# Performance work log

Hardware: AMD Instinct MI355X
Metric: run time of the kernel (lower is better)

The kernel has to match this reference:

```python
import jax, jax.numpy as jnp
import numpy as np

NUM_HEADS = 16
LN_EPS = 1e-5


def setup_inputs() -> dict:
    key = jax.random.key(0)
    ks = jax.random.split(key, 6)
    b, s, d = 2, 2048, 1024
    scale = 1.0 / np.sqrt(d)
    return {
        "x": jax.random.normal(ks[0], (b, s, d), dtype=jnp.float32),
        "W_w": jax.random.normal(ks[1], (3 * d, d), dtype=jnp.float32) * scale,
        "W_b": jax.random.normal(ks[2], (3 * d,), dtype=jnp.float32) * 0.01,
        "proj_w": jax.random.normal(ks[3], (d, d), dtype=jnp.float32) * scale,
        "proj_b": jax.random.normal(ks[4], (d,), dtype=jnp.float32) * 0.01,
        "gamma": jnp.ones((d,), dtype=jnp.float32),
        "beta": jnp.zeros((d,), dtype=jnp.float32),
    }


def reference(x, W_w, W_b, proj_w, proj_b, gamma, beta):
    b, s, d = x.shape
    h = NUM_HEADS
    hd = d // h
    # fused QKV projection: [b,s,3d]
    qkv = x @ W_w.T + W_b
    q, k, v = jnp.split(qkv, 3, axis=-1)
    # [b,s,d] -> [b,h,s,hd]
    q, k, v = (z.reshape(b, s, h, hd).transpose(0, 2, 1, 3) for z in (q, k, v))
    # NOTE: original scales by sqrt(d), not sqrt(head_dim)
    attn = jnp.einsum('bhqd,bhkd->bhqk', q, k) / jnp.sqrt(jnp.asarray(d, x.dtype))
    attn_weights = jax.nn.softmax(attn, axis=-1)  # [b,h,s,s]
    o = jnp.einsum('bhqk,bhkd->bhqd', attn_weights, v)
    o = o.transpose(0, 2, 1, 3).reshape(b, s, d)
    out = o @ proj_w.T + proj_b  # dropout is identity at eval
    y = x + out
    mu = jnp.mean(y, axis=-1, keepdims=True)
    var = jnp.var(y, axis=-1, keepdims=True)
    y_norm = (y - mu) / jnp.sqrt(var + LN_EPS) * gamma + beta
    return (y_norm, attn_weights)
```

## Files before the change

### kernel.cpp

```cpp
#include <hip/hip_runtime.h>
#include <cstdint>

#define BB 2
#define SS 2048
#define DD 1024
#define HH 16
#define HDIM 64
#define MM (BB*SS)
#define N3 (3*DD)

typedef __attribute__((ext_vector_type(4))) float f32x4;
typedef __attribute__((ext_vector_type(8))) __bf16 bf16x8;

static __device__ __forceinline__ unsigned short f2bf_fast(float f) {
  __bf16 h = (__bf16)f;
  return __builtin_bit_cast(unsigned short, h);
}

static __device__ __forceinline__ uint4 pack8f(const float4 a, const float4 b) {
  union { unsigned short us[8]; uint4 v; } pk;
  pk.us[0] = f2bf_fast(a.x); pk.us[1] = f2bf_fast(a.y); pk.us[2] = f2bf_fast(a.z); pk.us[3] = f2bf_fast(a.w);
  pk.us[4] = f2bf_fast(b.x); pk.us[5] = f2bf_fast(b.y); pk.us[6] = f2bf_fast(b.z); pk.us[7] = f2bf_fast(b.w);
  return pk.v;
}

static __device__ __forceinline__ void gload16(const unsigned short* g, unsigned short* l) {
  __builtin_amdgcn_global_load_lds(
      (const __attribute__((address_space(1))) void*)g,
      (__attribute__((address_space(3))) void*)l, 16, 0, 0);
}

__global__ __launch_bounds__(256) void cvt_kernel(
    const float* __restrict__ x, const float* __restrict__ Ww,
    const float* __restrict__ pw,
    unsigned short* __restrict__ xb, unsigned short* __restrict__ Wwb,
    unsigned short* __restrict__ pwb) {
  const size_t i = ((size_t)blockIdx.x * 256 + threadIdx.x) * 8;
  const float* src;
  unsigned short* dst;
  if (i < 4194304u)       { src = x  + i;            dst = xb  + i; }
  else if (i < 7340032u)  { src = Ww + (i - 4194304u); dst = Wwb + (i - 4194304u); }
  else                    { src = pw + (i - 7340032u); dst = pwb + (i - 7340032u); }
  const float4* s4 = (const float4*)src;
  *(uint4*)dst = pack8f(s4[0], s4[1]);
}

__global__ __launch_bounds__(256) void gemm_qkv(
    const unsigned short* __restrict__ xb, const unsigned short* __restrict__ Wwb,
    const float* __restrict__ Wb,
    unsigned short* __restrict__ qb, unsigned short* __restrict__ kb,
    unsigned short* __restrict__ vbT) {
  __shared__ __align__(16) unsigned short Sh[128 * 132];
  unsigned short* As = Sh;
  unsigned short* Bs = Sh + 128 * 32;
  const int t = threadIdx.x;
  const int l = t & 63, w = t >> 6;
  const int wr = w >> 1, wc = w & 1;
  const int m0 = blockIdx.y * 128, n0 = blockIdx.x * 128;
  f32x4 acc[4][4] = {};

  for (int kt = 0; kt < DD; kt += 32) {
    __syncthreads();
    #pragma unroll
    for (int i = 0; i < 2; ++i) {
      const int row = (i * 4 + w) * 16 + (l >> 2);
      const int cc = (l & 3) * 8;
      gload16(xb  + (size_t)(m0 + row) * DD + kt + cc, &As[(i * 4 + w) * 512]);
      gload16(Wwb + (size_t)(n0 + row) * DD + kt + cc, &Bs[(i * 4 + w) * 512]);
    }
    __syncthreads();
    bf16x8 a[4], b[4];
    #pragma unroll
    for (int i = 0; i < 4; ++i) {
      a[i] = __builtin_bit_cast(bf16x8, *(const uint4*)&As[(wr * 64 + i * 16 + (l & 15)) * 32 + (l >> 4) * 8]);
      b[i] = __builtin_bit_cast(bf16x8, *(const uint4*)&Bs[(wc * 64 + i * 16 + (l & 15)) * 32 + (l >> 4) * 8]);
    }
    #pragma unroll
    for (int i = 0; i < 4; ++i)
      #pragma unroll
      for (int j = 0; j < 4; ++j)
        acc[i][j] = __builtin_amdgcn_mfma_f32_16x16x32_bf16(a[i], b[j], acc[i][j], 0, 0, 0);
  }
  __syncthreads();

  if (n0 < 2048) {
    const bool isq = (n0 < 1024);
    #pragma unroll
    for (int i = 0; i < 4; ++i)
      #pragma unroll
      for (int j = 0; j < 4; ++j)
        #pragma unroll
        for (int r = 0; r < 4; ++r) {
          const int row = m0 + wr * 64 + i * 16 + (l >> 4) * 4 + r;
          const int col = n0 + wc * 64 + j * 16 + (l & 15);
          const float v = acc[i][j][r] + Wb[col];
          const int bidx = row >> 11, srow = row & 2047;
          const int cc = col & 1023, head = cc >> 6, hd = cc & 63;
          const size_t idx = ((size_t)((bidx * HH + head) * SS + srow)) * HDIM + hd;
          if (isq) qb[idx] = f2bf_fast(v * 0.04508422f);
          else     kb[idx] = f2bf_fast(v);
        }
  } else {
    unsigned short* Tt = Sh;
    #pragma unroll
    for (int i = 0; i < 4; ++i)
      #pragma unroll
      for (int j = 0; j < 4; ++j)
        #pragma unroll
        for (int r = 0; r < 4; ++r) {
          const int rr = wr * 64 + i * 16 + (l >> 4) * 4 + r;
          const int cl = wc * 64 + j * 16 + (l & 15);
          Tt[rr * 132 + cl] = f2bf_fast(acc[i][j][r] + Wb[n0 + cl]);
        }
    __syncthreads();
    const int bidx = m0 >> 11, srow0 = m0 & 2047;
    const int q = t & 3;
    #pragma unroll
    for (int ci = 0; ci < 2; ++ci) {
      const int c = ci * 64 + (t >> 2);
      const int vcol = n0 - 2048 + c;
      const int head = vcol >> 6, hd = vcol & 63;
      unsigned short* dst = vbT + ((size_t)(bidx * HH + head) * HDIM + hd) * SS + srow0;
      #pragma unroll
      for (int e8 = 0; e8 < 4; ++e8) {
        const int r0 = e8 * 32 + q * 8;
        union { unsigned short us[8]; uint4 v; } pk;
        #pragma unroll
        for (int e = 0; e < 8; ++e) pk.us[e] = Tt[(r0 + e) * 132 + c];
        *(uint4*)(dst + r0) = pk.v;
      }
    }
  }
}

__global__ __launch_bounds__(256) void attn_kernel(
    const unsigned short* __restrict__ qb,
    const unsigned short* __restrict__ kb,
    const unsigned short* __restrict__ vbT,
    unsigned short* __restrict__ ob,
    float* __restrict__ attn_out) {
  __shared__ float Ored[4][64][68];
  __shared__ float Lred[4][64];
  const int t = threadIdx.x;
  const int l = t & 63, w = t >> 6;
  const int q_l = l & 15, hi = l >> 4;
  const int bid = blockIdx.x;
  const int swz = (bid & 7) * 128 + (bid >> 3);
  const int bh = swz >> 5;
  const int q0 = (swz & 31) * 64;
  const size_t base = (size_t)bh * SS * HDIM;

  bf16x8 qa[4][2];
  #pragma unroll
  for (int j = 0; j < 4; ++j)
    #pragma unroll
    for (int kc = 0; kc < 2; ++kc)
      qa[j][kc] = __builtin_bit_cast(bf16x8,
          *(const uint4*)(qb + base + (size_t)(q0 + j * 16 + q_l) * HDIM + kc * 32 + hi * 8));

  const unsigned short* kga = kb + base + (size_t)(w * 16 + q_l) * HDIM + hi * 8;
  const unsigned short* vga = vbT + ((size_t)bh * HDIM + q_l) * SS + w * 16 + hi * 4;

  float lsum[4] = {0.f, 0.f, 0.f, 0.f};
  {
    uint4 k0 = *(const uint4*)(kga);
    uint4 k1 = *(const uint4*)(kga + 32);
    for (int kt = 0; kt < SS; kt += 64) {
      const bool more = (kt + 64) < SS;
      uint4 n0, n1;
      if (more) {
        n0 = *(const uint4*)(kga + (size_t)(kt + 64) * HDIM);
        n1 = *(const uint4*)(kga + (size_t)(kt + 64) * HDIM + 32);
      }
      f32x4 sQ[4] = {};
      const bf16x8 kf0 = __builtin_bit_cast(bf16x8, k0);
      const bf16x8 kf1 = __builtin_bit_cast(bf16x8, k1);
      __builtin_amdgcn_s_setprio(1);
      #pragma unroll
      for (int j = 0; j < 4; ++j) {
        sQ[j] = __builtin_amdgcn_mfma_f32_16x16x32_bf16(kf0, qa[j][0], sQ[j], 0, 0, 0);
        sQ[j] = __builtin_amdgcn_mfma_f32_16x16x32_bf16(kf1, qa[j][1], sQ[j], 0, 0, 0);
      }
      __builtin_amdgcn_s_setprio(0);
      #pragma unroll
      for (int j = 0; j < 4; ++j)
        #pragma unroll
        for (int r = 0; r < 4; ++r)
          lsum[j] += __builtin_amdgcn_exp2f(sQ[j][r]);
      k0 = n0; k1 = n1;
    }
  }
  #pragma unroll
  for (int j = 0; j < 4; ++j) {
    float s = lsum[j];
    s += __shfl_xor(s, 16);
    s += __shfl_xor(s, 32);
    lsum[j] = s;
  }
  if (hi == 0) {
    #pragma unroll
    for (int j = 0; j < 4; ++j) Lred[w][j * 16 + q_l] = lsum[j];
  }
  __syncthreads();
  float rl[4];
  #pragma unroll
  for (int j = 0; j < 4; ++j)
    rl[j] = 1.0f / (Lred[0][j * 16 + q_l] + Lred[1][j * 16 + q_l] +
                    Lred[2][j * 16 + q_l] + Lred[3][j * 16 + q_l]);

  float* pbs[4];
  #pragma unroll
  for (int j = 0; j < 4; ++j)
    pbs[j] = attn_out + ((size_t)bh * SS + (q0 + j * 16 + q_l)) * SS + w * 16 + hi * 4;

  f32x4 of[4][4] = {};
  {
    uint4 k0 = *(const uint4*)(kga);
    uint4 k1 = *(const uint4*)(kga + 32);
    uint2 vv[4];
    #pragma unroll
    for (int d4 = 0; d4 < 4; ++d4)
      vv[d4] = *(const uint2*)(vga + (size_t)(d4 * 16) * SS);
    for (int kt = 0; kt < SS; kt += 64) {
      const bool more = (kt + 64) < SS;
      uint4 n0, n1; uint2 nv[4];
      if (more) {
        n0 = *(const uint4*)(kga + (size_t)(kt + 64) * HDIM);
        n1 = *(const uint4*)(kga + (size_t)(kt + 64) * HDIM + 32);
        #pragma unroll
        for (int d4 = 0; d4 < 4; ++d4)
          nv[d4] = *(const uint2*)(vga + (size_t)(d4 * 16) * SS + kt + 64);
      }
      f32x4 sQ[4] = {};
      const bf16x8 kf0 = __builtin_bit_cast(bf16x8, k0);
      const bf16x8 kf1 = __builtin_bit_cast(bf16x8, k1);
      __builtin_amdgcn_s_setprio(1);
      #pragma unroll
      for (int j = 0; j < 4; ++j) {
        sQ[j] = __builtin_amdgcn_mfma_f32_16x16x32_bf16(kf0, qa[j][0], sQ[j], 0, 0, 0);
        sQ[j] = __builtin_amdgcn_mfma_f32_16x16x32_bf16(kf1, qa[j][1], sQ[j], 0, 0, 0);
      }
      __builtin_amdgcn_s_setprio(0);
      bf16x8 pbp[4];
      #pragma unroll
      for (int j = 0; j < 4; ++j) {
        float4 pv;
        pv.x = __builtin_amdgcn_exp2f(sQ[j][0]) * rl[j];
        pv.y = __builtin_amdgcn_exp2f(sQ[j][1]) * rl[j];
        pv.z = __builtin_amdgcn_exp2f(sQ[j][2]) * rl[j];
        pv.w = __builtin_amdgcn_exp2f(sQ[j][3]) * rl[j];
        __builtin_nontemporal_store(*(const f32x4*)&pv, (f32x4*)(pbs[j] + kt));
        union { unsigned short us[8]; uint4 v; } pk;
        pk.us[0] = f2bf_fast(pv.x); pk.us[1] = f2bf_fast(pv.y);
        pk.us[2] = f2bf_fast(pv.z); pk.us[3] = f2bf_fast(pv.w);
        pk.us[4] = 0; pk.us[5] = 0; pk.us[6] = 0; pk.us[7] = 0;
        pbp[j] = __builtin_bit_cast(bf16x8, pk.v);
      }
      __builtin_amdgcn_s_setprio(1);
      #pragma unroll
      for (int d4 = 0; d4 < 4; ++d4) {
        uint4 vp; vp.x = vv[d4].x; vp.y = vv[d4].y; vp.z = 0u; vp.w = 0u;
        const bf16x8 vfp = __builtin_bit_cast(bf16x8, vp);
        #pragma unroll
        for (int j = 0; j < 4; ++j)
          of[d4][j] = __builtin_amdgcn_mfma_f32_16x16x32_bf16(vfp, pbp[j], of[d4][j], 0, 0, 0);
      }
      __builtin_amdgcn_s_setprio(0);
      k0 = n0; k1 = n1;
      #pragma unroll
      for (int d4 = 0; d4 < 4; ++d4) vv[d4] = nv[d4];
    }
  }

  #pragma unroll
  for (int d4 = 0; d4 < 4; ++d4)
    #pragma unroll
    for (int j = 0; j < 4; ++j)
      *(f32x4*)&Ored[w][j * 16 + q_l][d4 * 16 + hi * 4] = of[d4][j];
  __syncthreads();
  const int bidx = bh >> 4, h_ = bh & 15;
  const int qf = w * 16 + q_l;
  union { unsigned short us[16]; uint4 v[2]; } opk;
  #pragma unroll
  for (int c4 = 0; c4 < 4; ++c4) {
    const int d0 = hi * 16 + c4 * 4;
    f32x4 s = *(const f32x4*)&Ored[0][qf][d0];
    s += *(const f32x4*)&Ored[1][qf][d0];
    s += *(const f32x4*)&Ored[2][qf][d0];
    s += *(const f32x4*)&Ored[3][qf][d0];
    opk.us[c4 * 4 + 0] = f2bf_fast(s[0]);
    opk.us[c4 * 4 + 1] = f2bf_fast(s[1]);
    opk.us[c4 * 4 + 2] = f2bf_fast(s[2]);
    opk.us[c4 * 4 + 3] = f2bf_fast(s[3]);
  }
  unsigned short* orow = ob + ((size_t)bidx * SS + (q0 + qf)) * DD + h_ * 64 + hi * 16;
  *(uint4*)orow = opk.v[0];
  *(uint4*)(orow + 8) = opk.v[1];
}

__global__ __launch_bounds__(256) void gemm_proj(
    const unsigned short* __restrict__ ob, const unsigned short* __restrict__ pwb,
    const float* __restrict__ pb, const float* __restrict__ x,
    float* __restrict__ y) {
  __shared__ __align__(16) unsigned short As[64 * 32];
  __shared__ __align__(16) unsigned short Bs[128 * 32];
  const int t = threadIdx.x;
  const int l = t & 63, w = t >> 6;
  const int wr = w >> 1, wc = w & 1;
  const int m0 = blockIdx.y * 64, n0 = blockIdx.x * 128;
  f32x4 acc[2][4] = {};

  for (int kt = 0; kt < DD; kt += 32) {
    __syncthreads();
    {
      const int rowA = w * 16 + (l >> 2);
      const int cc = (l & 3) * 8;
      gload16(ob + (size_t)(m0 + rowA) * DD + kt + cc, &As[w * 512]);
      #pragma unroll
      for (int i = 0; i < 2; ++i) {
        const int rowB = (i * 4 + w) * 16 + (l >> 2);
        gload16(pwb + (size_t)(n0 + rowB) * DD + kt + cc, &Bs[(i * 4 + w) * 512]);
      }
    }
    __syncthreads();
    bf16x8 a[2], b[4];
    #pragma unroll
    for (int i = 0; i < 2; ++i)
      a[i] = __builtin_bit_cast(bf16x8, *(const uint4*)&As[(wr * 32 + i * 16 + (l & 15)) * 32 + (l >> 4) * 8]);
    #pragma unroll
    for (int j = 0; j < 4; ++j)
      b[j] = __builtin_bit_cast(bf16x8, *(const uint4*)&Bs[(wc * 64 + j * 16 + (l & 15)) * 32 + (l >> 4) * 8]);
    #pragma unroll
    for (int i = 0; i < 2; ++i)
      #pragma unroll
      for (int j = 0; j < 4; ++j)
        acc[i][j] = __builtin_amdgcn_mfma_f32_16x16x32_bf16(a[i], b[j], acc[i][j], 0, 0, 0);
  }
  #pragma unroll
  for (int i = 0; i < 2; ++i)
    #pragma unroll
    for (int j = 0; j < 4; ++j)
      #pragma unroll
      for (int r = 0; r < 4; ++r) {
        const int row = m0 + wr * 32 + i * 16 + (l >> 4) * 4 + r;
        const int col = n0 + wc * 64 + j * 16 + (l & 15);
        const size_t idx = (size_t)row * DD + col;
        y[idx] = acc[i][j][r] + pb[col] + x[idx];
      }
}

__global__ __launch_bounds__(256) void ln_kernel(
    float* __restrict__ y, const float* __restrict__ gamma,
    const float* __restrict__ beta) {
  const int row = blockIdx.x;
  const int t = threadIdx.x;
  const float4 v = ((const float4*)(y + (size_t)row * DD))[t];
  float s  = v.x + v.y + v.z + v.w;
  float s2 = v.x * v.x + v.y * v.y + v.z * v.z + v.w * v.w;
  #pragma unroll
  for (int off = 1; off < 64; off <<= 1) { s += __shfl_xor(s, off); s2 += __shfl_xor(s2, off); }
  __shared__ float red[8];
  const int l = t & 63, w = t >> 6;
  if (l == 0) { red[w] = s; red[4 + w] = s2; }
  __syncthreads();
  s  = red[0] + red[1] + red[2] + red[3];
  s2 = red[4] + red[5] + red[6] + red[7];
  const float mu = s * (1.0f / DD);
  const float var = s2 * (1.0f / DD) - mu * mu;
  const float rs = rsqrtf(var + 1e-5f);
  const float4 g  = ((const float4*)gamma)[t];
  const float4 be = ((const float4*)beta)[t];
  float4 o;
  o.x = (v.x - mu) * rs * g.x + be.x;
  o.y = (v.y - mu) * rs * g.y + be.y;
  o.z = (v.z - mu) * rs * g.z + be.z;
  o.w = (v.w - mu) * rs * g.w + be.w;
  ((float4*)(y + (size_t)row * DD))[t] = o;
}

extern "C" void kernel_launch(void* const* d_in, const int* in_sizes, int n_in,
                              void* d_out, int out_size, void* d_ws, size_t ws_size,
                              hipStream_t stream) {
  const float* x     = (const float*)d_in[0];
  const float* Ww    = (const float*)d_in[1];
  const float* Wb    = (const float*)d_in[2];
  const float* Pw    = (const float*)d_in[3];
  const float* Pb    = (const float*)d_in[4];
  const float* gamma = (const float*)d_in[5];
  const float* beta  = (const float*)d_in[6];

  float* out      = (float*)d_out;
  float* y_norm   = out;
  float* attn_out = out + (size_t)MM * DD;

  char* ws = (char*)d_ws;
  unsigned short* qb  = (unsigned short*)(ws);
  unsigned short* kb  = (unsigned short*)(ws +  8388608);
  unsigned short* vbT = (unsigned short*)(ws + 16777216);
  unsigned short* ob  = (unsigned short*)(ws + 25165824);
  unsigned short* xb  = (unsigned short*)(ws + 33554432);
  unsigned short* Wwb = (unsigned short*)(ws + 41943040);
  unsigned short* pwb = (unsigned short*)(ws + 48234496);

  cvt_kernel<<<4096, 256, 0, stream>>>(x, Ww, Pw, xb, Wwb, pwb);
  gemm_qkv<<<dim3(N3 / 128, MM / 128), 256, 0, stream>>>(xb, Wwb, Wb, qb, kb, vbT);
  attn_kernel<<<1024, 256, 0, stream>>>(qb, kb, vbT, ob, attn_out);
  gemm_proj<<<dim3(DD / 128, MM / 64), 256, 0, stream>>>(ob, pwb, Pb, x, y_norm);
  ln_kernel<<<MM, 256, 0, stream>>>(y_norm, gamma, beta);
}
```

Before: 260.4 us.

## Raise attention kernel occupancy by halving LDS and dropping register prefetch

Adds a min-blocks hint of 3 to the attention kernel's launch bounds. It halves the shared reduction buffer by reducing the output in two halves of 32 rows. It also removes the software prefetch of the next K/V tile from both key loops, which frees registers. The aim is more resident blocks per CU so memory latency is hidden by other waves rather than by explicit prefetch. The risk is exposed load latency per iteration, possible spilling under the tighter register budget, and an extra barrier round in the epilogue.

```diff
diff --git a/kernel.cpp b/kernel.cpp
--- a/kernel.cpp
+++ b/kernel.cpp
@@ -133,13 +133,13 @@
   }
 }
 
-__global__ __launch_bounds__(256) void attn_kernel(
+__global__ __launch_bounds__(256, 3) void attn_kernel(
     const unsigned short* __restrict__ qb,
     const unsigned short* __restrict__ kb,
     const unsigned short* __restrict__ vbT,
     unsigned short* __restrict__ ob,
     float* __restrict__ attn_out) {
-  __shared__ float Ored[4][64][68];
+  __shared__ float Ored[4][32][68];
   __shared__ float Lred[4][64];
   const int t = threadIdx.x;
   const int l = t & 63, w = t >> 6;
@@ -162,33 +162,24 @@
   const unsigned short* vga = vbT + ((size_t)bh * HDIM + q_l) * SS + w * 16 + hi * 4;
 
   float lsum[4] = {0.f, 0.f, 0.f, 0.f};
-  {
-    uint4 k0 = *(const uint4*)(kga);
-    uint4 k1 = *(const uint4*)(kga + 32);
-    for (int kt = 0; kt < SS; kt += 64) {
-      const bool more = (kt + 64) < SS;
-      uint4 n0, n1;
-      if (more) {
-        n0 = *(const uint4*)(kga + (size_t)(kt + 64) * HDIM);
-        n1 = *(const uint4*)(kga + (size_t)(kt + 64) * HDIM + 32);
-      }
-      f32x4 sQ[4] = {};
-      const bf16x8 kf0 = __builtin_bit_cast(bf16x8, k0);
-      const bf16x8 kf1 = __builtin_bit_cast(bf16x8, k1);
-      __builtin_amdgcn_s_setprio(1);
-      #pragma unroll
-      for (int j = 0; j < 4; ++j) {
-        sQ[j] = __builtin_amdgcn_mfma_f32_16x16x32_bf16(kf0, qa[j][0], sQ[j], 0, 0, 0);
-        sQ[j] = __builtin_amdgcn_mfma_f32_16x16x32_bf16(kf1, qa[j][1], sQ[j], 0, 0, 0);
-      }
-      __builtin_amdgcn_s_setprio(0);
-      #pragma unroll
-      for (int j = 0; j < 4; ++j)
-        #pragma unroll
-        for (int r = 0; r < 4; ++r)
-          lsum[j] += __builtin_amdgcn_exp2f(sQ[j][r]);
-      k0 = n0; k1 = n1;
-    }
+  for (int kt = 0; kt < SS; kt += 64) {
+    const uint4 k0 = *(const uint4*)(kga + (size_t)kt * HDIM);
+    const uint4 k1 = *(const uint4*)(kga + (size_t)kt * HDIM + 32);
+    f32x4 sQ[4] = {};
+    const bf16x8 kf0 = __builtin_bit_cast(bf16x8, k0);
+    const bf16x8 kf1 = __builtin_bit_cast(bf16x8, k1);
+    __builtin_amdgcn_s_setprio(1);
+    #pragma unroll
+    for (int j = 0; j < 4; ++j) {
+      sQ[j] = __builtin_amdgcn_mfma_f32_16x16x32_bf16(kf0, qa[j][0], sQ[j], 0, 0, 0);
+      sQ[j] = __builtin_amdgcn_mfma_f32_16x16x32_bf16(kf1, qa[j][1], sQ[j], 0, 0, 0);
+    }
+    __builtin_amdgcn_s_setprio(0);
+    #pragma unroll
+    for (int j = 0; j < 4; ++j)
+      #pragma unroll
+      for (int r = 0; r < 4; ++r)
+        lsum[j] += __builtin_amdgcn_exp2f(sQ[j][r]);
   }
   #pragma unroll
   for (int j = 0; j < 4; ++j) {
@@ -214,88 +205,86 @@
     pbs[j] = attn_out + ((size_t)bh * SS + (q0 + j * 16 + q_l)) * SS + w * 16 + hi * 4;
 
   f32x4 of[4][4] = {};
+  for (int kt = 0; kt < SS; kt += 64) {
+    const uint4 k0 = *(const uint4*)(kga + (size_t)kt * HDIM);
+    const uint4 k1 = *(const uint4*)(kga + (size_t)kt * HDIM + 32);
+    uint2 vv[4];
+    #pragma unroll
+    for (int d4 = 0; d4 < 4; ++d4)
+      vv[d4] = *(const uint2*)(vga + (size_t)(d4 * 16) * SS + kt);
+    f32x4 sQ[4] = {};
+    const bf16x8 kf0 = __builtin_bit_cast(bf16x8, k0);
+    const bf16x8 kf1 = __builtin_bit_cast(bf16x8, k1);
+    __builtin_amdgcn_s_setprio(1);
+    #pragma unroll
+    for (int j = 0; j < 4; ++j) {
+      sQ[j] = __builtin_amdgcn_mfma_f32_16x16x32_bf16(kf0, qa[j][0], sQ[j], 0, 0, 0);
+      sQ[j] = __builtin_amdgcn_mfma_f32_16x16x32_bf16(kf1, qa[j][1], sQ[j], 0, 0, 0);
+    }
+    __builtin_amdgcn_s_setprio(0);
+    bf16x8 pbp[4];
+    #pragma unroll
+    for (int j = 0; j < 4; ++j) {
+      float4 pv;
+      pv.x = __builtin_amdgcn_exp2f(sQ[j][0]) * rl[j];
+      pv.y = __builtin_amdgcn_exp2f(sQ[j][1]) * rl[j];
+      pv.z = __builtin_amdgcn_exp2f(sQ[j][2]) * rl[j];
+      pv.w = __builtin_amdgcn_exp2f(sQ[j][3]) * rl[j];
+      __builtin_nontemporal_store(*(const f32x4*)&pv, (f32x4*)(pbs[j] + kt));
+      union { unsigned short us[8]; uint4 v; } pk;
+      pk.us[0] = f2bf_fast(pv.x); pk.us[1] = f2bf_fast(pv.y);
+      pk.us[2] = f2bf_fast(pv.z); pk.us[3] = f2bf_fast(pv.w);
+      pk.us[4] = 0; pk.us[5] = 0; pk.us[6] = 0; pk.us[7] = 0;
+      pbp[j] = __builtin_bit_cast(bf16x8, pk.v);
+    }
+    __builtin_amdgcn_s_setprio(1);
+    #pragma unroll
+    for (int d4 = 0; d4 < 4; ++d4) {
+      uint4 vp; vp.x = vv[d4].x; vp.y = vv[d4].y; vp.z = 0u; vp.w = 0u;
+      const bf16x8 vfp = __builtin_bit_cast(bf16x8, vp);
+      #pragma unroll
+      for (int j = 0; j < 4; ++j)
+        of[d4][j] = __builtin_amdgcn_mfma_f32_16x16x32_bf16(vfp, pbp[j], of[d4][j], 0, 0, 0);
+    }
+    __builtin_amdgcn_s_setprio(0);
+  }
+
+  const int bidx = bh >> 4, h_ = bh & 15;
+  const int row = t >> 3, seg = t & 7;
+  const int d0 = seg * 8;
+  #pragma unroll
+  for (int d4 = 0; d4 < 4; ++d4)
+    #pragma unroll
+    for (int j = 0; j < 2; ++j)
+      *(f32x4*)&Ored[w][j * 16 + q_l][d4 * 16 + hi * 4] = of[d4][j];
+  __syncthreads();
   {
-    uint4 k0 = *(const uint4*)(kga);
-    uint4 k1 = *(const uint4*)(kga + 32);
-    uint2 vv[4];
-    #pragma unroll
-    for (int d4 = 0; d4 < 4; ++d4)
-      vv[d4] = *(const uint2*)(vga + (size_t)(d4 * 16) * SS);
-    for (int kt = 0; kt < SS; kt += 64) {
-      const bool more = (kt + 64) < SS;
-      uint4 n0, n1; uint2 nv[4];
-      if (more) {
-        n0 = *(const uint4*)(kga + (size_t)(kt + 64) * HDIM);
-        n1 = *(const uint4*)(kga + (size_t)(kt + 64) * HDIM + 32);
-        #pragma unroll
-        for (int d4 = 0; d4 < 4; ++d4)
-          nv[d4] = *(const uint2*)(vga + (size_t)(d4 * 16) * SS + kt + 64);
-      }
-      f32x4 sQ[4] = {};
-      const bf16x8 kf0 = __builtin_bit_cast(bf16x8, k0);
-      const bf16x8 kf1 = __builtin_bit_cast(bf16x8, k1);
-      __builtin_amdgcn_s_setprio(1);
-      #pragma unroll
-      for (int j = 0; j < 4; ++j) {
-        sQ[j] = __builtin_amdgcn_mfma_f32_16x16x32_bf16(kf0, qa[j][0], sQ[j], 0, 0, 0);
-        sQ[j] = __builtin_amdgcn_mfma_f32_16x16x32_bf16(kf1, qa[j][1], sQ[j], 0, 0, 0);
-      }
-      __builtin_amdgcn_s_setprio(0);
-      bf16x8 pbp[4];
-      #pragma unroll
-      for (int j = 0; j < 4; ++j) {
-        float4 pv;
-        pv.x = __builtin_amdgcn_exp2f(sQ[j][0]) * rl[j];
-        pv.y = __builtin_amdgcn_exp2f(sQ[j][1]) * rl[j];
-        pv.z = __builtin_amdgcn_exp2f(sQ[j][2]) * rl[j];
-        pv.w = __builtin_amdgcn_exp2f(sQ[j][3]) * rl[j];
-        __builtin_nontemporal_store(*(const f32x4*)&pv, (f32x4*)(pbs[j] + kt));
-        union { unsigned short us[8]; uint4 v; } pk;
-        pk.us[0] = f2bf_fast(pv.x); pk.us[1] = f2bf_fast(pv.y);
-        pk.us[2] = f2bf_fast(pv.z); pk.us[3] = f2bf_fast(pv.w);
-        pk.us[4] = 0; pk.us[5] = 0; pk.us[6] = 0; pk.us[7] = 0;
-        pbp[j] = __builtin_bit_cast(bf16x8, pk.v);
-      }
-      __builtin_amdgcn_s_setprio(1);
-      #pragma unroll
-      for (int d4 = 0; d4 < 4; ++d4) {
-        uint4 vp; vp.x = vv[d4].x; vp.y = vv[d4].y; vp.z = 0u; vp.w = 0u;
-        const bf16x8 vfp = __builtin_bit_cast(bf16x8, vp);
-        #pragma unroll
-        for (int j = 0; j < 4; ++j)
-          of[d4][j] = __builtin_amdgcn_mfma_f32_16x16x32_bf16(vfp, pbp[j], of[d4][j], 0, 0, 0);
-      }
-      __builtin_amdgcn_s_setprio(0);
-      k0 = n0; k1 = n1;
-      #pragma unroll
-      for (int d4 = 0; d4 < 4; ++d4) vv[d4] = nv[d4];
-    }
-  }
-
+    union { unsigned short us[8]; uint4 v; } opk;
+    #pragma unroll
+    for (int e = 0; e < 8; ++e) {
+      const float s = Ored[0][row][d0 + e] + Ored[1][row][d0 + e] +
+                      Ored[2][row][d0 + e] + Ored[3][row][d0 + e];
+      opk.us[e] = f2bf_fast(s);
+    }
+    *(uint4*)(ob + ((size_t)bidx * SS + (q0 + row)) * DD + h_ * 64 + d0) = opk.v;
+  }
+  __syncthreads();
   #pragma unroll
   for (int d4 = 0; d4 < 4; ++d4)
     #pragma unroll
-    for (int j = 0; j < 4; ++j)
-      *(f32x4*)&Ored[w][j * 16 + q_l][d4 * 16 + hi * 4] = of[d4][j];
-  __syncthreads();
-  const int bidx = bh >> 4, h_ = bh & 15;
-  const int qf = w * 16 + q_l;
-  union { unsigned short us[16]; uint4 v[2]; } opk;
-  #pragma unroll
-  for (int c4 = 0; c4 < 4; ++c4) {
-    const int d0 = hi * 16 + c4 * 4;
-    f32x4 s = *(const f32x4*)&Ored[0][qf][d0];
-    s += *(const f32x4*)&Ored[1][qf][d0];
-    s += *(const f32x4*)&Ored[2][qf][d0];
-    s += *(const f32x4*)&Ored[3][qf][d0];
-    opk.us[c4 * 4 + 0] = f2bf_fast(s[0]);
-    opk.us[c4 * 4 + 1] = f2bf_fast(s[1]);
-    opk.us[c4 * 4 + 2] = f2bf_fast(s[2]);
-    opk.us[c4 * 4 + 3] = f2bf_fast(s[3]);
-  }
-  unsigned short* orow = ob + ((size_t)bidx * SS + (q0 + qf)) * DD + h_ * 64 + hi * 16;
-  *(uint4*)orow = opk.v[0];
-  *(uint4*)(orow + 8) = opk.v[1];
+    for (int j = 2; j < 4; ++j)
+      *(f32x4*)&Ored[w][(j - 2) * 16 + q_l][d4 * 16 + hi * 4] = of[d4][j];
+  __syncthreads();
+  {
+    union { unsigned short us[8]; uint4 v; } opk;
+    #pragma unroll
+    for (int e = 0; e < 8; ++e) {
+      const float s = Ored[0][row][d0 + e] + Ored[1][row][d0 + e] +
+                      Ored[2][row][d0 + e] + Ored[3][row][d0 + e];
+      opk.us[e] = f2bf_fast(s);
+    }
+    *(uint4*)(ob + ((size_t)bidx * SS + (q0 + 32 + row)) * DD + h_ * 64 + d0) = opk.v;
+  }
 }
 
 __global__ __launch_bounds__(256) void gemm_proj(
```

Measured after the change: 260.9 us. No clear change (+0.2%).

## Process two 64-key tiles per iteration to fill zero-padded PV MFMA

Applied to the files above, without the earlier changes.

The attention loop now handles 128 keys per iteration. Two score tiles are packed into the upper and lower halves of the 32-wide K dimension of the PV MFMA, where the upper half was previously zero padding. This halves the number of PV MFMA instructions, which were wasting half their work. In exchange, the explicit register prefetch of the next K/V tile is removed, so load latency is now exposed and has to be hidden by occupancy or the compiler.

```diff
diff --git a/kernel.cpp b/kernel.cpp
--- a/kernel.cpp
+++ b/kernel.cpp
@@ -214,62 +214,57 @@
     pbs[j] = attn_out + ((size_t)bh * SS + (q0 + j * 16 + q_l)) * SS + w * 16 + hi * 4;
 
   f32x4 of[4][4] = {};
-  {
-    uint4 k0 = *(const uint4*)(kga);
-    uint4 k1 = *(const uint4*)(kga + 32);
-    uint2 vv[4];
-    #pragma unroll
-    for (int d4 = 0; d4 < 4; ++d4)
-      vv[d4] = *(const uint2*)(vga + (size_t)(d4 * 16) * SS);
-    for (int kt = 0; kt < SS; kt += 64) {
-      const bool more = (kt + 64) < SS;
-      uint4 n0, n1; uint2 nv[4];
-      if (more) {
-        n0 = *(const uint4*)(kga + (size_t)(kt + 64) * HDIM);
-        n1 = *(const uint4*)(kga + (size_t)(kt + 64) * HDIM + 32);
-        #pragma unroll
-        for (int d4 = 0; d4 < 4; ++d4)
-          nv[d4] = *(const uint2*)(vga + (size_t)(d4 * 16) * SS + kt + 64);
-      }
-      f32x4 sQ[4] = {};
-      const bf16x8 kf0 = __builtin_bit_cast(bf16x8, k0);
-      const bf16x8 kf1 = __builtin_bit_cast(bf16x8, k1);
-      __builtin_amdgcn_s_setprio(1);
-      #pragma unroll
-      for (int j = 0; j < 4; ++j) {
-        sQ[j] = __builtin_amdgcn_mfma_f32_16x16x32_bf16(kf0, qa[j][0], sQ[j], 0, 0, 0);
-        sQ[j] = __builtin_amdgcn_mfma_f32_16x16x32_bf16(kf1, qa[j][1], sQ[j], 0, 0, 0);
-      }
-      __builtin_amdgcn_s_setprio(0);
-      bf16x8 pbp[4];
-      #pragma unroll
-      for (int j = 0; j < 4; ++j) {
-        float4 pv;
-        pv.x = __builtin_amdgcn_exp2f(sQ[j][0]) * rl[j];
-        pv.y = __builtin_amdgcn_exp2f(sQ[j][1]) * rl[j];
-        pv.z = __builtin_amdgcn_exp2f(sQ[j][2]) * rl[j];
-        pv.w = __builtin_amdgcn_exp2f(sQ[j][3]) * rl[j];
-        __builtin_nontemporal_store(*(const f32x4*)&pv, (f32x4*)(pbs[j] + kt));
-        union { unsigned short us[8]; uint4 v; } pk;
-        pk.us[0] = f2bf_fast(pv.x); pk.us[1] = f2bf_fast(pv.y);
-        pk.us[2] = f2bf_fast(pv.z); pk.us[3] = f2bf_fast(pv.w);
-        pk.us[4] = 0; pk.us[5] = 0; pk.us[6] = 0; pk.us[7] = 0;
-        pbp[j] = __builtin_bit_cast(bf16x8, pk.v);
-      }
-      __builtin_amdgcn_s_setprio(1);
-      #pragma unroll
-      for (int d4 = 0; d4 < 4; ++d4) {
-        uint4 vp; vp.x = vv[d4].x; vp.y = vv[d4].y; vp.z = 0u; vp.w = 0u;
-        const bf16x8 vfp = __builtin_bit_cast(bf16x8, vp);
-        #pragma unroll
-        for (int j = 0; j < 4; ++j)
-          of[d4][j] = __builtin_amdgcn_mfma_f32_16x16x32_bf16(vfp, pbp[j], of[d4][j], 0, 0, 0);
-      }
-      __builtin_amdgcn_s_setprio(0);
-      k0 = n0; k1 = n1;
-      #pragma unroll
-      for (int d4 = 0; d4 < 4; ++d4) vv[d4] = nv[d4];
-    }
+  for (int kt = 0; kt < SS; kt += 128) {
+    const uint4 k0 = *(const uint4*)(kga + (size_t)kt * HDIM);
+    const uint4 k1 = *(const uint4*)(kga + (size_t)kt * HDIM + 32);
+    const uint4 k2 = *(const uint4*)(kga + (size_t)(kt + 64) * HDIM);
+    const uint4 k3 = *(const uint4*)(kga + (size_t)(kt + 64) * HDIM + 32);
+    uint2 vv0[4], vv1[4];
+    #pragma unroll
+    for (int d4 = 0; d4 < 4; ++d4) {
+      vv0[d4] = *(const uint2*)(vga + (size_t)(d4 * 16) * SS + kt);
+      vv1[d4] = *(const uint2*)(vga + (size_t)(d4 * 16) * SS + kt + 64);
+    }
+    const bf16x8 kf0 = __builtin_bit_cast(bf16x8, k0);
+    const bf16x8 kf1 = __builtin_bit_cast(bf16x8, k1);
+    const bf16x8 kf2 = __builtin_bit_cast(bf16x8, k2);
+    const bf16x8 kf3 = __builtin_bit_cast(bf16x8, k3);
+    f32x4 sQa[4] = {}, sQb[4] = {};
+    __builtin_amdgcn_s_setprio(1);
+    #pragma unroll
+    for (int j = 0; j < 4; ++j) {
+      sQa[j] = __builtin_amdgcn_mfma_f32_16x16x32_bf16(kf0, qa[j][0], sQa[j], 0, 0, 0);
+      sQa[j] = __builtin_amdgcn_mfma_f32_16x16x32_bf16(kf1, qa[j][1], sQa[j], 0, 0, 0);
+      sQb[j] = __builtin_amdgcn_mfma_f32_16x16x32_bf16(kf2, qa[j][0], sQb[j], 0, 0, 0);
+      sQb[j] = __builtin_amdgcn_mfma_f32_16x16x32_bf16(kf3, qa[j][1], sQb[j], 0, 0, 0);
+    }
+    __builtin_amdgcn_s_setprio(0);
+    bf16x8 pbp[4];
+    #pragma unroll
+    for (int j = 0; j < 4; ++j) {
+      float4 pva, pvb;
+      pva.x = __builtin_amdgcn_exp2f(sQa[j][0]) * rl[j];
+      pva.y = __builtin_amdgcn_exp2f(sQa[j][1]) * rl[j];
+      pva.z = __builtin_amdgcn_exp2f(sQa[j][2]) * rl[j];
+      pva.w = __builtin_amdgcn_exp2f(sQa[j][3]) * rl[j];
+      pvb.x = __builtin_amdgcn_exp2f(sQb[j][0]) * rl[j];
+      pvb.y = __builtin_amdgcn_exp2f(sQb[j][1]) * rl[j];
+      pvb.z = __builtin_amdgcn_exp2f(sQb[j][2]) * rl[j];
+      pvb.w = __builtin_amdgcn_exp2f(sQb[j][3]) * rl[j];
+      __builtin_nontemporal_store(*(const f32x4*)&pva, (f32x4*)(pbs[j] + kt));
+      __builtin_nontemporal_store(*(const f32x4*)&pvb, (f32x4*)(pbs[j] + kt + 64));
+      pbp[j] = __builtin_bit_cast(bf16x8, pack8f(pva, pvb));
+    }
+    __builtin_amdgcn_s_setprio(1);
+    #pragma unroll
+    for (int d4 = 0; d4 < 4; ++d4) {
+      uint4 vp; vp.x = vv0[d4].x; vp.y = vv0[d4].y; vp.z = vv1[d4].x; vp.w = vv1[d4].y;
+      const bf16x8 vfp = __builtin_bit_cast(bf16x8, vp);
+      #pragma unroll
+      for (int j = 0; j < 4; ++j)
+        of[d4][j] = __builtin_amdgcn_mfma_f32_16x16x32_bf16(vfp, pbp[j], of[d4][j], 0, 0, 0);
+    }
+    __builtin_amdgcn_s_setprio(0);
   }
 
   #pragma unroll
```

Result: faster. 247.8 us (-4.8%).
